# Kernel tuning notes

Hardware: AMD Instinct MI355X
Metric: run time of the kernel (lower is better)

Reference implementation:

```python
import jax, jax.numpy as jnp
import numpy as np

# Model dims
H = 1024          # hidden_size
I = 2048          # intermediate_size
E = 8             # num_experts
IE = I // E       # expert_intermediate_size = 256
V = 100000        # vocab_size
B, S = 8, 2048


def _rowwise_quantize(x):
    """Dynamic per-row int8 quantization (faithful to dynamic_quantize_int8, per_channel=True).
    Returns quantized values kept in float32 (identical values to int8->float cast) and per-row scale."""
    max_vals = jnp.max(jnp.abs(x), axis=-1, keepdims=True)
    scale = jnp.maximum(max_vals / 127.0, 1e-8)
    x_q = jnp.clip(jnp.round(x / scale), -128.0, 127.0)
    return x_q, scale[..., 0]


def _quantize_weight(w):
    """Per-output-channel int8 quantization of a [K, N] weight (as in from_float)."""
    max_vals = jnp.max(jnp.abs(w), axis=0, keepdims=True)      # [1, N]
    scale = jnp.maximum(max_vals / 127.0, 1e-8)
    w_q = jnp.clip(jnp.round(w / scale), -128.0, 127.0).astype(jnp.int8)
    return w_q, scale[0]


def setup_inputs() -> dict:
    key = jax.random.key(0)
    ks = jax.random.split(key, 6)
    hidden_states = jax.random.normal(ks[0], (B, S, H), dtype=jnp.float32)
    token_ids = jax.random.randint(ks[1], (B, S), 0, V, dtype=jnp.int32)

    # Pre-quantized expert weights (int8) with per-output-channel fp32 scales.
    gate_w = jax.random.normal(ks[2], (E, H, IE), dtype=jnp.float32) * 0.02
    up_w = jax.random.normal(ks[3], (E, H, IE), dtype=jnp.float32) * 0.02
    down_w = jax.random.normal(ks[4], (E, IE, H), dtype=jnp.float32) * 0.02
    gate_q, gate_scale = jax.vmap(_quantize_weight)(gate_w)   # [E,H,IE] int8, [E,IE]
    up_q, up_scale = jax.vmap(_quantize_weight)(up_w)         # [E,H,IE] int8, [E,IE]
    down_q, down_scale = jax.vmap(_quantize_weight)(down_w)   # [E,IE,H] int8, [E,H]

    # Deterministic contiguous token->expert mapping (V divisible by E here).
    token_to_expert = jnp.minimum(jnp.arange(V, dtype=jnp.int32) // (V // E), E - 1)

    return {
        "hidden_states": hidden_states,
        "token_ids": token_ids,
        "gate_q": gate_q, "gate_scale": gate_scale,
        "up_q": up_q, "up_scale": up_scale,
        "down_q": down_q, "down_scale": down_scale,
        "token_to_expert": token_to_expert,
    }


def reference(hidden_states, token_ids, gate_q, gate_scale, up_q, up_scale,
              down_q, down_scale, token_to_expert):
    Bh, Sh, Hh = hidden_states.shape
    n_exp = gate_q.shape[0]
    vocab = token_to_expert.shape[0]

    tid = jnp.clip(token_ids, 0, vocab - 1)
    expert_ids = token_to_expert[tid].reshape(-1)             # [T]

    x = hidden_states.reshape(-1, Hh)                          # [T, H]
    # Per-row activation quantization is expert-independent -> do it once for all tokens.
    x_q, x_s = _rowwise_quantize(x)                            # [T,H], [T]

    gq = gate_q.astype(jnp.float32)
    uq = up_q.astype(jnp.float32)
    dq = down_q.astype(jnp.float32)

    out = jnp.zeros_like(x)
    for e in range(n_exp):  # small fixed expert count
        # fused quantize-GEMM: int8 matmul + per-row activation scale + per-col weight scale
        gate = (x_q @ gq[e]) * x_s[:, None] * gate_scale[e][None, :]   # [T, IE]
        up = (x_q @ uq[e]) * x_s[:, None] * up_scale[e][None, :]       # [T, IE]
        inter = jax.nn.silu(gate) * up
        i_q, i_s = _rowwise_quantize(inter)
        o = (i_q @ dq[e]) * i_s[:, None] * down_scale[e][None, :]      # [T, H]
        out = jnp.where((expert_ids == e)[:, None], o, out)
    return out.reshape(Bh, Sh, Hh)
```

## Files before the change

kernel.cpp:

```cpp
#include <hip/hip_runtime.h>
#include <hip/hip_bf16.h>

typedef int   int4v   __attribute__((ext_vector_type(4)));
typedef float float4v __attribute__((ext_vector_type(4)));

#define T_TOK 16384
#define TPAD  16448
#define HD    1024
#define IE    256
#define EN    8
#define VSZ   100000

#define M_OFF 16
#define M_TS1 25
#define M_TS2 34

#define XQ_OFF   0ull
#define IQ_OFF   16842752ull
#define PB1_OFF  21053440ull
#define PB2_OFF  25247744ull
#define PERM_OFF 27344896ull
#define XS_OFF   27410688ull
#define IS_OFF   27476480ull
#define META_OFF 27542272ull
#define BC_OFF   27542528ull
#define BB_OFF   27544576ull

__global__ void k_hist(const int* __restrict__ ids, const int* __restrict__ t2e,
                       int* __restrict__ bc) {
    __shared__ int h[EN];
    if (threadIdx.x < EN) h[threadIdx.x] = 0;
    __syncthreads();
    int t = blockIdx.x * 256 + threadIdx.x;
    int id = ids[t]; id = min(max(id, 0), VSZ - 1);
    atomicAdd(&h[t2e[id]], 1);
    __syncthreads();
    if (threadIdx.x < EN) bc[blockIdx.x * EN + threadIdx.x] = h[threadIdx.x];
}

__global__ __launch_bounds__(512) void k_scan(const int* __restrict__ bc,
                                              int* __restrict__ bbase,
                                              int* __restrict__ meta) {
    int e = threadIdx.x >> 6;
    int b = threadIdx.x & 63;
    int c = bc[b * EN + e];
    int inc = c;
    #pragma unroll
    for (int s = 1; s < 64; s <<= 1) {
        int v = __shfl_up(inc, s, 64);
        if (b >= s) inc += v;
    }
    int exc = inc - c;
    __shared__ int tot[EN];
    __shared__ int goff[EN];
    if (b == 63) tot[e] = inc;
    __syncthreads();
    if (threadIdx.x == 0) {
        int off = 0, t1 = 0, t2 = 0;
        meta[M_OFF] = 0; meta[M_TS1] = 0; meta[M_TS2] = 0;
        #pragma unroll
        for (int i = 0; i < EN; ++i) {
            goff[i] = off;
            int cc = tot[i];
            off += cc; t1 += (cc + 63) >> 6; t2 += (cc + 31) >> 5;
            meta[M_OFF + i + 1] = off;
            meta[M_TS1 + i + 1] = t1;
            meta[M_TS2 + i + 1] = t2;
        }
    }
    __syncthreads();
    bbase[b * EN + e] = goff[e] + exc;
}

__global__ void k_assign(const int* __restrict__ ids, const int* __restrict__ t2e,
                         const int* __restrict__ bbase, int* __restrict__ perm) {
    __shared__ int cur[EN];
    if (threadIdx.x < EN) cur[threadIdx.x] = bbase[blockIdx.x * EN + threadIdx.x];
    __syncthreads();
    int t = blockIdx.x * 256 + threadIdx.x;
    int id = ids[t]; id = min(max(id, 0), VSZ - 1);
    int e = t2e[id];
    int slot = atomicAdd(&cur[e], 1);
    perm[slot] = t;
}

__global__ __launch_bounds__(256) void k_repack(const int* __restrict__ gq,
                                                const int* __restrict__ uq,
                                                const int* __restrict__ dq,
                                                signed char* __restrict__ pb1,
                                                signed char* __restrict__ pb2) {
    int idx = blockIdx.x * 256 + threadIdx.x;
    if (idx < 262144) {
        int n = idx & 511, kc = (idx >> 9) & 63, e = idx >> 15;
        const int* src = (n < 256) ? gq + (((size_t)((e << 10) + (kc << 4)) << 8) + n)
                                   : uq + (((size_t)((e << 10) + (kc << 4)) << 8) + (n - 256));
        int4v pk;
        #pragma unroll
        for (int jj = 0; jj < 4; ++jj) {
            int b0 = src[(size_t)(jj * 4 + 0) << 8], b1 = src[(size_t)(jj * 4 + 1) << 8];
            int b2 = src[(size_t)(jj * 4 + 2) << 8], b3 = src[(size_t)(jj * 4 + 3) << 8];
            pk[jj] = (b0 & 255) | ((b1 & 255) << 8) | ((b2 & 255) << 16) | (b3 << 24);
        }
        *(int4v*)(pb1 + ((size_t)((((e << 6) + kc) << 9) + n) << 4)) = pk;
    } else {
        int j = idx - 262144;
        int n = j & 1023, kc = (j >> 10) & 15, e = j >> 14;
        const int* src = dq + (((size_t)((e << 8) + (kc << 4)) << 10) + n);
        int4v pk;
        #pragma unroll
        for (int jj = 0; jj < 4; ++jj) {
            int b0 = src[(size_t)(jj * 4 + 0) << 10], b1 = src[(size_t)(jj * 4 + 1) << 10];
            int b2 = src[(size_t)(jj * 4 + 2) << 10], b3 = src[(size_t)(jj * 4 + 3) << 10];
            pk[jj] = (b0 & 255) | ((b1 & 255) << 8) | ((b2 & 255) << 16) | (b3 << 24);
        }
        *(int4v*)(pb2 + ((size_t)((((e << 4) + kc) << 10) + n) << 4)) = pk;
    }
}

__global__ __launch_bounds__(256) void k_quant(const float* __restrict__ hidden,
                                               const int* __restrict__ perm,
                                               signed char* __restrict__ xq,
                                               float* __restrict__ xs) {
    int w = threadIdx.x >> 6, lane = threadIdx.x & 63;
    int slot = blockIdx.x * 4 + w;
    int token = perm[slot];
    const float* row = hidden + (size_t)token * HD;
    float v[16];
    #pragma unroll
    for (int j = 0; j < 4; ++j) {
        float4v f = *(const float4v*)(row + lane * 16 + j * 4);
        v[j*4+0] = f[0]; v[j*4+1] = f[1]; v[j*4+2] = f[2]; v[j*4+3] = f[3];
    }
    float mx = 0.0f;
    #pragma unroll
    for (int j = 0; j < 16; ++j) mx = fmaxf(mx, fabsf(v[j]));
    #pragma unroll
    for (int s = 1; s < 64; s <<= 1) mx = fmaxf(mx, __shfl_xor(mx, s, 64));
    float sc = fmaxf(mx / 127.0f, 1e-8f);
    if (lane == 0) xs[slot] = sc;
    int4v pk;
    #pragma unroll
    for (int j = 0; j < 4; ++j) {
        int b[4];
        #pragma unroll
        for (int u = 0; u < 4; ++u) {
            float t = rintf(v[j*4+u] / sc);
            t = fminf(fmaxf(t, -128.0f), 127.0f);
            b[u] = (int)t;
        }
        pk[j] = (b[0] & 255) | ((b[1] & 255) << 8) | ((b[2] & 255) << 16) | (b[3] << 24);
    }
    *(int4v*)(xq + (size_t)slot * HD + lane * 16) = pk;
}

__global__ __launch_bounds__(256) void k_gemm1(const signed char* __restrict__ xq,
                                               const signed char* __restrict__ pb1,
                                               const float* __restrict__ xs,
                                               const float* __restrict__ gsc,
                                               const float* __restrict__ usc,
                                               const int* __restrict__ meta,
                                               signed char* __restrict__ iq,
                                               float* __restrict__ isc) {
    int b = blockIdx.x;
    int e = -1, m0 = 0, gend = 0;
    #pragma unroll
    for (int i = 0; i < EN; ++i) {
        int s0 = meta[M_TS1 + i], s1 = meta[M_TS1 + i + 1];
        if (b >= s0 && b < s1) { e = i; m0 = meta[M_OFF + i] + ((b - s0) << 6); gend = meta[M_OFF + i + 1]; }
    }
    if (e < 0) return;
    const int w = threadIdx.x >> 6, lane = threadIdx.x & 63;
    const int q = lane >> 4, r = lane & 15;

    int4v zero = {0, 0, 0, 0};
    int4v accg[4][4], accu[4][4];
    #pragma unroll
    for (int mi = 0; mi < 4; ++mi)
        #pragma unroll
        for (int i = 0; i < 4; ++i) { accg[mi][i] = zero; accu[mi][i] = zero; }

    const signed char* pbe = pb1 + (size_t)e * (64 * 512 * 16);
    for (int k0 = 0; k0 < HD; k0 += 64) {
        int4v a[4];
        #pragma unroll
        for (int mi = 0; mi < 4; ++mi)
            a[mi] = *(const int4v*)(xq + (size_t)(m0 + mi * 16 + r) * HD + k0 + q * 16);
        int kc = (k0 >> 4) + q;
        #pragma unroll
        for (int i = 0; i < 4; ++i) {
            int n = w * 64 + i * 16 + r;
            int4v bg = *(const int4v*)(pbe + (((size_t)kc * 512 + n) << 4));
            int4v bu = *(const int4v*)(pbe + (((size_t)kc * 512 + n + 256) << 4));
            #pragma unroll
            for (int mi = 0; mi < 4; ++mi) {
                accg[mi][i] = __builtin_amdgcn_mfma_i32_16x16x64_i8(a[mi], bg, accg[mi][i], 0, 0, 0);
                accu[mi][i] = __builtin_amdgcn_mfma_i32_16x16x64_i8(a[mi], bu, accu[mi][i], 0, 0, 0);
            }
        }
    }

    float gs[4], us[4];
    #pragma unroll
    for (int i = 0; i < 4; ++i) {
        int n = w * 64 + i * 16 + r;
        gs[i] = gsc[e * IE + n];
        us[i] = usc[e * IE + n];
    }
    float xsr[4][4];
    #pragma unroll
    for (int mi = 0; mi < 4; ++mi)
        #pragma unroll
        for (int g = 0; g < 4; ++g)
            xsr[mi][g] = xs[m0 + mi * 16 + q * 4 + g];

    float inter[4][4][4];
    float pm[4][4];
    #pragma unroll
    for (int mi = 0; mi < 4; ++mi)
        #pragma unroll
        for (int g = 0; g < 4; ++g) {
            float mx = 0.0f;
            #pragma unroll
            for (int i = 0; i < 4; ++i) {
                float gv = (float)accg[mi][i][g] * xsr[mi][g] * gs[i];
                float uv = (float)accu[mi][i][g] * xsr[mi][g] * us[i];
                float sg = gv / (1.0f + expf(-gv));
                float vv = sg * uv;
                inter[mi][i][g] = vv;
                mx = fmaxf(mx, fabsf(vv));
            }
            #pragma unroll
            for (int s = 1; s < 16; s <<= 1) mx = fmaxf(mx, __shfl_xor(mx, s, 64));
            pm[mi][g] = mx;
        }

    __shared__ float pmax[4][64];
    __shared__ float rsc[64];
    if (r == 0) {
        #pragma unroll
        for (int mi = 0; mi < 4; ++mi)
            #pragma unroll
            for (int g = 0; g < 4; ++g)
                pmax[w][mi * 16 + q * 4 + g] = pm[mi][g];
    }
    __syncthreads();
    if (threadIdx.x < 64) {
        int row = threadIdx.x;
        float mx = fmaxf(fmaxf(pmax[0][row], pmax[1][row]), fmaxf(pmax[2][row], pmax[3][row]));
        float sc = fmaxf(mx / 127.0f, 1e-8f);
        rsc[row] = sc;
        if (m0 + row < gend) isc[m0 + row] = sc;
    }
    __syncthreads();
    #pragma unroll
    for (int mi = 0; mi < 4; ++mi)
        #pragma unroll
        for (int g = 0; g < 4; ++g) {
            int row = mi * 16 + q * 4 + g;
            int slot = m0 + row;
            if (slot < gend) {
                float sc = rsc[row];
                #pragma unroll
                for (int i = 0; i < 4; ++i) {
                    float t = rintf(inter[mi][i][g] / sc);
                    t = fminf(fmaxf(t, -128.0f), 127.0f);
                    iq[(size_t)slot * IE + w * 64 + i * 16 + r] = (signed char)(int)t;
                }
            }
        }
}

__global__ __launch_bounds__(256) void k_gemm2(const signed char* __restrict__ iq,
                                               const signed char* __restrict__ pb2,
                                               const float* __restrict__ isc,
                                               const float* __restrict__ dsc,
                                               const int* __restrict__ meta,
                                               const int* __restrict__ perm,
                                               float* __restrict__ out) {
    int b = blockIdx.x;
    int e = -1, m0 = 0, gend = 0;
    #pragma unroll
    for (int i = 0; i < EN; ++i) {
        int s0 = meta[M_TS2 + i], s1 = meta[M_TS2 + i + 1];
        if (b >= s0 && b < s1) { e = i; m0 = meta[M_OFF + i] + ((b - s0) << 5); gend = meta[M_OFF + i + 1]; }
    }
    if (e < 0) return;
    const int w = threadIdx.x >> 6, lane = threadIdx.x & 63;
    const int q = lane >> 4, r = lane & 15;

    int4v zero = {0, 0, 0, 0};
    int4v acc[2][16];
    #pragma unroll
    for (int mi = 0; mi < 2; ++mi)
        #pragma unroll
        for (int i = 0; i < 16; ++i) acc[mi][i] = zero;

    const signed char* pbe = pb2 + (size_t)e * (16 * 1024 * 16);
    for (int k0 = 0; k0 < IE; k0 += 64) {
        int4v a[2];
        #pragma unroll
        for (int mi = 0; mi < 2; ++mi)
            a[mi] = *(const int4v*)(iq + (size_t)(m0 + mi * 16 + r) * IE + k0 + q * 16);
        int kc = (k0 >> 4) + q;
        #pragma unroll
        for (int i = 0; i < 16; ++i) {
            int n = w * 256 + i * 16 + r;
            int4v bb = *(const int4v*)(pbe + (((size_t)kc * 1024 + n) << 4));
            acc[0][i] = __builtin_amdgcn_mfma_i32_16x16x64_i8(a[0], bb, acc[0][i], 0, 0, 0);
            acc[1][i] = __builtin_amdgcn_mfma_i32_16x16x64_i8(a[1], bb, acc[1][i], 0, 0, 0);
        }
    }

    float ds[16];
    #pragma unroll
    for (int i = 0; i < 16; ++i)
        ds[i] = dsc[e * HD + w * 256 + i * 16 + r];
    float isr[2][4]; int tok[2][4];
    #pragma unroll
    for (int mi = 0; mi < 2; ++mi)
        #pragma unroll
        for (int g = 0; g < 4; ++g) {
            int slot = m0 + mi * 16 + q * 4 + g;
            isr[mi][g] = isc[slot];
            tok[mi][g] = perm[slot];
        }
    #pragma unroll
    for (int mi = 0; mi < 2; ++mi)
        #pragma unroll
        for (int g = 0; g < 4; ++g) {
            int slot = m0 + mi * 16 + q * 4 + g;
            if (slot < gend) {
                float vs = isr[mi][g];
                size_t ob = (size_t)tok[mi][g] * HD + w * 256 + r;
                #pragma unroll
                for (int i = 0; i < 16; ++i)
                    out[ob + i * 16] = (float)acc[mi][i][g] * vs * ds[i];
            }
        }
}

extern "C" void kernel_launch(void* const* d_in, const int* in_sizes, int n_in,
                              void* d_out, int out_size, void* d_ws, size_t ws_size,
                              hipStream_t stream) {
    const float* hidden = (const float*)d_in[0];
    const int*   ids    = (const int*)d_in[1];
    const int*   gq     = (const int*)d_in[2];
    const float* gsc    = (const float*)d_in[3];
    const int*   uq     = (const int*)d_in[4];
    const float* usc    = (const float*)d_in[5];
    const int*   dq     = (const int*)d_in[6];
    const float* dsc    = (const float*)d_in[7];
    const int*   t2e    = (const int*)d_in[8];
    float* out = (float*)d_out;

    char* ws = (char*)d_ws;
    signed char* xq  = (signed char*)(ws + XQ_OFF);
    signed char* iq  = (signed char*)(ws + IQ_OFF);
    signed char* pb1 = (signed char*)(ws + PB1_OFF);
    signed char* pb2 = (signed char*)(ws + PB2_OFF);
    int*   perm = (int*)(ws + PERM_OFF);
    float* xs   = (float*)(ws + XS_OFF);
    float* isc  = (float*)(ws + IS_OFF);
    int*   meta = (int*)(ws + META_OFF);
    int*   bc   = (int*)(ws + BC_OFF);
    int*   bbase= (int*)(ws + BB_OFF);

    k_hist<<<64, 256, 0, stream>>>(ids, t2e, bc);
    k_scan<<<1, 512, 0, stream>>>(bc, bbase, meta);
    k_assign<<<64, 256, 0, stream>>>(ids, t2e, bbase, perm);
    k_repack<<<1536, 256, 0, stream>>>(gq, uq, dq, pb1, pb2);
    k_quant<<<4096, 256, 0, stream>>>(hidden, perm, xq, xs);
    k_gemm1<<<264, 256, 0, stream>>>(xq, pb1, xs, gsc, usc, meta, iq, isc);
    k_gemm2<<<520, 256, 0, stream>>>(iq, pb2, isc, dsc, meta, perm, out);
}
```

Baseline: 249.4 us.

## Stage GEMM operands through double-buffered LDS via direct global-to-LDS loads

After: 211.4 us. 15.2% less time.

```diff
diff --git a/kernel.cpp b/kernel.cpp
--- a/kernel.cpp
+++ b/kernel.cpp
@@ -25,6 +25,13 @@
 #define META_OFF 27542272ull
 #define BC_OFF   27542528ull
 #define BB_OFF   27544576ull
+
+__device__ __forceinline__ void gload16(const void* g, void* l) {
+    __builtin_amdgcn_global_load_lds(
+        (const __attribute__((address_space(1))) unsigned int*)g,
+        (__attribute__((address_space(3))) unsigned int*)l,
+        16, 0, 0);
+}
 
 __global__ void k_hist(const int* __restrict__ ids, const int* __restrict__ t2e,
                        int* __restrict__ bc) {
@@ -153,14 +160,14 @@
     *(int4v*)(xq + (size_t)slot * HD + lane * 16) = pk;
 }
 
-__global__ __launch_bounds__(256) void k_gemm1(const signed char* __restrict__ xq,
-                                               const signed char* __restrict__ pb1,
-                                               const float* __restrict__ xs,
-                                               const float* __restrict__ gsc,
-                                               const float* __restrict__ usc,
-                                               const int* __restrict__ meta,
-                                               signed char* __restrict__ iq,
-                                               float* __restrict__ isc) {
+__global__ __launch_bounds__(256, 2) void k_gemm1(const signed char* __restrict__ xq,
+                                                  const signed char* __restrict__ pb1,
+                                                  const float* __restrict__ xs,
+                                                  const float* __restrict__ gsc,
+                                                  const float* __restrict__ usc,
+                                                  const int* __restrict__ meta,
+                                                  signed char* __restrict__ iq,
+                                                  float* __restrict__ isc) {
     int b = blockIdx.x;
     int e = -1, m0 = 0, gend = 0;
     #pragma unroll
@@ -172,6 +179,28 @@
     const int w = threadIdx.x >> 6, lane = threadIdx.x & 63;
     const int q = lane >> 4, r = lane & 15;
 
+    __shared__ signed char lB[2][32768];
+    __shared__ signed char lA[2][4096];
+    __shared__ float pmax[4][64];
+    __shared__ float rsc[64];
+
+    const signed char* pbe = pb1 + (size_t)e * (64 * 512 * 16);
+    const int arow = (w << 4) + (lane >> 2);
+    const int acq  = (lane & 3) ^ ((lane >> 2) & 3);
+    const signed char* ga_base = xq + (size_t)(m0 + arow) * HD + (acq << 4);
+
+    #define G1_STAGE(buf, kt)                                                          \
+        {                                                                              \
+            int kc0 = (kt) << 2;                                                       \
+            _Pragma("unroll")                                                          \
+            for (int j = 0; j < 8; ++j) {                                              \
+                int n = ((j << 6) + lane) ^ ((w & 1) << 3);                            \
+                gload16(pbe + (((size_t)(kc0 + w) * 512 + n) << 4),                    \
+                        &lB[buf][((w << 3) + j) << 10]);                               \
+            }                                                                          \
+            gload16(ga_base + ((kt) << 6), &lA[buf][w << 10]);                         \
+        }
+
     int4v zero = {0, 0, 0, 0};
     int4v accg[4][4], accu[4][4];
     #pragma unroll
@@ -179,30 +208,36 @@
         #pragma unroll
         for (int i = 0; i < 4; ++i) { accg[mi][i] = zero; accu[mi][i] = zero; }
 
-    const signed char* pbe = pb1 + (size_t)e * (64 * 512 * 16);
-    for (int k0 = 0; k0 < HD; k0 += 64) {
+    G1_STAGE(0, 0);
+    for (int kt = 0; kt < 16; ++kt) {
+        int cur = kt & 1;
+        if (kt < 15) G1_STAGE(cur ^ 1, kt + 1);
+        __syncthreads();
         int4v a[4];
         #pragma unroll
         for (int mi = 0; mi < 4; ++mi)
-            a[mi] = *(const int4v*)(xq + (size_t)(m0 + mi * 16 + r) * HD + k0 + q * 16);
-        int kc = (k0 >> 4) + q;
+            a[mi] = *(const int4v*)&lA[cur][(((mi << 4) + r) << 6) + ((q ^ (r & 3)) << 4)];
         #pragma unroll
         for (int i = 0; i < 4; ++i) {
-            int n = w * 64 + i * 16 + r;
-            int4v bg = *(const int4v*)(pbe + (((size_t)kc * 512 + n) << 4));
-            int4v bu = *(const int4v*)(pbe + (((size_t)kc * 512 + n + 256) << 4));
+            int n = (w << 6) + (i << 4) + r;
+            int sg = (q << 9) + (n ^ ((q & 1) << 3));
+            int su = (q << 9) + ((n + 256) ^ ((q & 1) << 3));
+            int4v bg = *(const int4v*)&lB[cur][sg << 4];
+            int4v bu = *(const int4v*)&lB[cur][su << 4];
             #pragma unroll
             for (int mi = 0; mi < 4; ++mi) {
                 accg[mi][i] = __builtin_amdgcn_mfma_i32_16x16x64_i8(a[mi], bg, accg[mi][i], 0, 0, 0);
                 accu[mi][i] = __builtin_amdgcn_mfma_i32_16x16x64_i8(a[mi], bu, accu[mi][i], 0, 0, 0);
             }
         }
-    }
+        __syncthreads();
+    }
+    #undef G1_STAGE
 
     float gs[4], us[4];
     #pragma unroll
     for (int i = 0; i < 4; ++i) {
-        int n = w * 64 + i * 16 + r;
+        int n = (w << 6) + (i << 4) + r;
         gs[i] = gsc[e * IE + n];
         us[i] = usc[e * IE + n];
     }
@@ -234,8 +269,6 @@
             pm[mi][g] = mx;
         }
 
-    __shared__ float pmax[4][64];
-    __shared__ float rsc[64];
     if (r == 0) {
         #pragma unroll
         for (int mi = 0; mi < 4; ++mi)
@@ -264,57 +297,82 @@
                 for (int i = 0; i < 4; ++i) {
                     float t = rintf(inter[mi][i][g] / sc);
                     t = fminf(fmaxf(t, -128.0f), 127.0f);
-                    iq[(size_t)slot * IE + w * 64 + i * 16 + r] = (signed char)(int)t;
+                    iq[(size_t)slot * IE + (w << 6) + (i << 4) + r] = (signed char)(int)t;
                 }
             }
         }
 }
 
-__global__ __launch_bounds__(256) void k_gemm2(const signed char* __restrict__ iq,
-                                               const signed char* __restrict__ pb2,
-                                               const float* __restrict__ isc,
-                                               const float* __restrict__ dsc,
-                                               const int* __restrict__ meta,
-                                               const int* __restrict__ perm,
-                                               float* __restrict__ out) {
-    int b = blockIdx.x;
+__global__ __launch_bounds__(256, 2) void k_gemm2(const signed char* __restrict__ iq,
+                                                  const signed char* __restrict__ pb2,
+                                                  const float* __restrict__ isc,
+                                                  const float* __restrict__ dsc,
+                                                  const int* __restrict__ meta,
+                                                  const int* __restrict__ perm,
+                                                  float* __restrict__ out) {
+    int tile = blockIdx.x >> 1, nh = blockIdx.x & 1;
     int e = -1, m0 = 0, gend = 0;
     #pragma unroll
     for (int i = 0; i < EN; ++i) {
         int s0 = meta[M_TS2 + i], s1 = meta[M_TS2 + i + 1];
-        if (b >= s0 && b < s1) { e = i; m0 = meta[M_OFF + i] + ((b - s0) << 5); gend = meta[M_OFF + i + 1]; }
+        if (tile >= s0 && tile < s1) { e = i; m0 = meta[M_OFF + i] + ((tile - s0) << 5); gend = meta[M_OFF + i + 1]; }
     }
     if (e < 0) return;
     const int w = threadIdx.x >> 6, lane = threadIdx.x & 63;
     const int q = lane >> 4, r = lane & 15;
 
+    __shared__ signed char lB[2][32768];
+    __shared__ signed char lA[2][2048];
+
+    const signed char* pbe = pb2 + (size_t)e * (16 * 1024 * 16);
+    const int arow = (w << 4) + (lane >> 2);
+    const int acq  = (lane & 3) ^ ((lane >> 2) & 3);
+    const signed char* ga_base = iq + (size_t)(m0 + arow) * IE + (acq << 4);
+
+    #define G2_STAGE(buf, kt)                                                          \
+        {                                                                              \
+            int kc0 = (kt) << 2;                                                       \
+            _Pragma("unroll")                                                          \
+            for (int j = 0; j < 8; ++j) {                                              \
+                int n = ((j << 6) + lane) ^ ((w & 1) << 3);                            \
+                gload16(pbe + (((size_t)(kc0 + w) * 1024 + (nh << 9) + n) << 4),       \
+                        &lB[buf][((w << 3) + j) << 10]);                               \
+            }                                                                          \
+            if (w < 2) gload16(ga_base + ((kt) << 6), &lA[buf][w << 10]);              \
+        }
+
     int4v zero = {0, 0, 0, 0};
-    int4v acc[2][16];
+    int4v acc[2][8];
     #pragma unroll
     for (int mi = 0; mi < 2; ++mi)
         #pragma unroll
-        for (int i = 0; i < 16; ++i) acc[mi][i] = zero;
-
-    const signed char* pbe = pb2 + (size_t)e * (16 * 1024 * 16);
-    for (int k0 = 0; k0 < IE; k0 += 64) {
+        for (int i = 0; i < 8; ++i) acc[mi][i] = zero;
+
+    G2_STAGE(0, 0);
+    for (int kt = 0; kt < 4; ++kt) {
+        int cur = kt & 1;
+        if (kt < 3) G2_STAGE(cur ^ 1, kt + 1);
+        __syncthreads();
         int4v a[2];
         #pragma unroll
         for (int mi = 0; mi < 2; ++mi)
-            a[mi] = *(const int4v*)(iq + (size_t)(m0 + mi * 16 + r) * IE + k0 + q * 16);
-        int kc = (k0 >> 4) + q;
-        #pragma unroll
-        for (int i = 0; i < 16; ++i) {
-            int n = w * 256 + i * 16 + r;
-            int4v bb = *(const int4v*)(pbe + (((size_t)kc * 1024 + n) << 4));
+            a[mi] = *(const int4v*)&lA[cur][(((mi << 4) + r) << 6) + ((q ^ (r & 3)) << 4)];
+        #pragma unroll
+        for (int i = 0; i < 8; ++i) {
+            int n = (w << 7) + (i << 4) + r;
+            int sb = (q << 9) + (n ^ ((q & 1) << 3));
+            int4v bb = *(const int4v*)&lB[cur][sb << 4];
             acc[0][i] = __builtin_amdgcn_mfma_i32_16x16x64_i8(a[0], bb, acc[0][i], 0, 0, 0);
             acc[1][i] = __builtin_amdgcn_mfma_i32_16x16x64_i8(a[1], bb, acc[1][i], 0, 0, 0);
         }
-    }
-
-    float ds[16];
-    #pragma unroll
-    for (int i = 0; i < 16; ++i)
-        ds[i] = dsc[e * HD + w * 256 + i * 16 + r];
+        __syncthreads();
+    }
+    #undef G2_STAGE
+
+    float ds[8];
+    #pragma unroll
+    for (int i = 0; i < 8; ++i)
+        ds[i] = dsc[e * HD + (nh << 9) + (w << 7) + (i << 4) + r];
     float isr[2][4]; int tok[2][4];
     #pragma unroll
     for (int mi = 0; mi < 2; ++mi)
@@ -331,10 +389,10 @@
             int slot = m0 + mi * 16 + q * 4 + g;
             if (slot < gend) {
                 float vs = isr[mi][g];
-                size_t ob = (size_t)tok[mi][g] * HD + w * 256 + r;
+                size_t ob = (size_t)tok[mi][g] * HD + (nh << 9) + (w << 7) + r;
                 #pragma unroll
-                for (int i = 0; i < 16; ++i)
-                    out[ob + i * 16] = (float)acc[mi][i][g] * vs * ds[i];
+                for (int i = 0; i < 8; ++i)
+                    out[ob + (i << 4)] = (float)acc[mi][i][g] * vs * ds[i];
             }
         }
 }
@@ -371,5 +429,5 @@
     k_repack<<<1536, 256, 0, stream>>>(gq, uq, dq, pb1, pb2);
     k_quant<<<4096, 256, 0, stream>>>(hidden, perm, xq, xs);
     k_gemm1<<<264, 256, 0, stream>>>(xq, pb1, xs, gsc, usc, meta, iq, isc);
-    k_gemm2<<<520, 256, 0, stream>>>(iq, pb2, isc, dsc, meta, perm, out);
-}
+    k_gemm2<<<1040, 256, 0, stream>>>(iq, pb2, isc, dsc, meta, perm, out);
+}
```

## Quantize tokens in natural order, gather in GEMM1, pipeline loads, split GEMM2 N

Applied to the files above, without the earlier changes.

Result: faster. 241.3 us (-3.2%).

```diff
diff --git a/kernel.cpp b/kernel.cpp
--- a/kernel.cpp
+++ b/kernel.cpp
@@ -118,12 +118,10 @@
 }
 
 __global__ __launch_bounds__(256) void k_quant(const float* __restrict__ hidden,
-                                               const int* __restrict__ perm,
                                                signed char* __restrict__ xq,
                                                float* __restrict__ xs) {
     int w = threadIdx.x >> 6, lane = threadIdx.x & 63;
-    int slot = blockIdx.x * 4 + w;
-    int token = perm[slot];
+    int token = blockIdx.x * 4 + w;
     const float* row = hidden + (size_t)token * HD;
     float v[16];
     #pragma unroll
@@ -137,7 +135,7 @@
     #pragma unroll
     for (int s = 1; s < 64; s <<= 1) mx = fmaxf(mx, __shfl_xor(mx, s, 64));
     float sc = fmaxf(mx / 127.0f, 1e-8f);
-    if (lane == 0) xs[slot] = sc;
+    if (lane == 0) xs[token] = sc;
     int4v pk;
     #pragma unroll
     for (int j = 0; j < 4; ++j) {
@@ -150,7 +148,7 @@
         }
         pk[j] = (b[0] & 255) | ((b[1] & 255) << 8) | ((b[2] & 255) << 16) | (b[3] << 24);
     }
-    *(int4v*)(xq + (size_t)slot * HD + lane * 16) = pk;
+    *(int4v*)(xq + (size_t)token * HD + lane * 16) = pk;
 }
 
 __global__ __launch_bounds__(256) void k_gemm1(const signed char* __restrict__ xq,
@@ -159,6 +157,7 @@
                                                const float* __restrict__ gsc,
                                                const float* __restrict__ usc,
                                                const int* __restrict__ meta,
+                                               const int* __restrict__ perm,
                                                signed char* __restrict__ iq,
                                                float* __restrict__ isc) {
     int b = blockIdx.x;
@@ -172,6 +171,26 @@
     const int w = threadIdx.x >> 6, lane = threadIdx.x & 63;
     const int q = lane >> 4, r = lane & 15;
 
+    const signed char* pbe = pb1 + (size_t)e * (64 * 512 * 16);
+    const signed char* arow[4];
+    #pragma unroll
+    for (int mi = 0; mi < 4; ++mi)
+        arow[mi] = xq + (size_t)perm[min(m0 + (mi << 4) + r, T_TOK - 1)] * HD + (q << 4);
+    const signed char* brow = pbe + (((size_t)q * 512 + (w << 6) + r) << 4);
+
+    int4v A[2][4], BG[2][4], BU[2][4];
+    #define G1_LOAD(buf, kt)                                                            \
+        {                                                                               \
+            _Pragma("unroll")                                                           \
+            for (int mi = 0; mi < 4; ++mi)                                              \
+                A[buf][mi] = *(const int4v*)(arow[mi] + ((kt) << 6));                   \
+            _Pragma("unroll")                                                           \
+            for (int i = 0; i < 4; ++i) {                                               \
+                BG[buf][i] = *(const int4v*)(brow + ((size_t)(kt) << 15) + (i << 8));   \
+                BU[buf][i] = *(const int4v*)(brow + ((size_t)(kt) << 15) + (i << 8) + 4096); \
+            }                                                                           \
+        }
+
     int4v zero = {0, 0, 0, 0};
     int4v accg[4][4], accu[4][4];
     #pragma unroll
@@ -179,30 +198,26 @@
         #pragma unroll
         for (int i = 0; i < 4; ++i) { accg[mi][i] = zero; accu[mi][i] = zero; }
 
-    const signed char* pbe = pb1 + (size_t)e * (64 * 512 * 16);
-    for (int k0 = 0; k0 < HD; k0 += 64) {
-        int4v a[4];
-        #pragma unroll
-        for (int mi = 0; mi < 4; ++mi)
-            a[mi] = *(const int4v*)(xq + (size_t)(m0 + mi * 16 + r) * HD + k0 + q * 16);
-        int kc = (k0 >> 4) + q;
+    G1_LOAD(0, 0);
+    #pragma unroll
+    for (int kt = 0; kt < 16; ++kt) {
+        int cur = kt & 1;
+        if (kt < 15) G1_LOAD(cur ^ 1, kt + 1);
         #pragma unroll
         for (int i = 0; i < 4; ++i) {
-            int n = w * 64 + i * 16 + r;
-            int4v bg = *(const int4v*)(pbe + (((size_t)kc * 512 + n) << 4));
-            int4v bu = *(const int4v*)(pbe + (((size_t)kc * 512 + n + 256) << 4));
             #pragma unroll
             for (int mi = 0; mi < 4; ++mi) {
-                accg[mi][i] = __builtin_amdgcn_mfma_i32_16x16x64_i8(a[mi], bg, accg[mi][i], 0, 0, 0);
-                accu[mi][i] = __builtin_amdgcn_mfma_i32_16x16x64_i8(a[mi], bu, accu[mi][i], 0, 0, 0);
+                accg[mi][i] = __builtin_amdgcn_mfma_i32_16x16x64_i8(A[cur][mi], BG[cur][i], accg[mi][i], 0, 0, 0);
+                accu[mi][i] = __builtin_amdgcn_mfma_i32_16x16x64_i8(A[cur][mi], BU[cur][i], accu[mi][i], 0, 0, 0);
             }
         }
     }
+    #undef G1_LOAD
 
     float gs[4], us[4];
     #pragma unroll
     for (int i = 0; i < 4; ++i) {
-        int n = w * 64 + i * 16 + r;
+        int n = (w << 6) + (i << 4) + r;
         gs[i] = gsc[e * IE + n];
         us[i] = usc[e * IE + n];
     }
@@ -210,8 +225,10 @@
     #pragma unroll
     for (int mi = 0; mi < 4; ++mi)
         #pragma unroll
-        for (int g = 0; g < 4; ++g)
-            xsr[mi][g] = xs[m0 + mi * 16 + q * 4 + g];
+        for (int g = 0; g < 4; ++g) {
+            int sl = min(m0 + mi * 16 + q * 4 + g, T_TOK - 1);
+            xsr[mi][g] = xs[perm[sl]];
+        }
 
     float inter[4][4][4];
     float pm[4][4];
@@ -264,7 +281,7 @@
                 for (int i = 0; i < 4; ++i) {
                     float t = rintf(inter[mi][i][g] / sc);
                     t = fminf(fmaxf(t, -128.0f), 127.0f);
-                    iq[(size_t)slot * IE + w * 64 + i * 16 + r] = (signed char)(int)t;
+                    iq[(size_t)slot * IE + (w << 6) + (i << 4) + r] = (signed char)(int)t;
                 }
             }
         }
@@ -277,44 +294,51 @@
                                                const int* __restrict__ meta,
                                                const int* __restrict__ perm,
                                                float* __restrict__ out) {
-    int b = blockIdx.x;
+    int tile = blockIdx.x >> 2, nt = blockIdx.x & 3;
     int e = -1, m0 = 0, gend = 0;
     #pragma unroll
     for (int i = 0; i < EN; ++i) {
         int s0 = meta[M_TS2 + i], s1 = meta[M_TS2 + i + 1];
-        if (b >= s0 && b < s1) { e = i; m0 = meta[M_OFF + i] + ((b - s0) << 5); gend = meta[M_OFF + i + 1]; }
+        if (tile >= s0 && tile < s1) { e = i; m0 = meta[M_OFF + i] + ((tile - s0) << 5); gend = meta[M_OFF + i + 1]; }
     }
     if (e < 0) return;
     const int w = threadIdx.x >> 6, lane = threadIdx.x & 63;
     const int q = lane >> 4, r = lane & 15;
 
+    const signed char* pbe = pb2 + (size_t)e * (16 * 1024 * 16);
+    const signed char* arow0 = iq + (size_t)(m0 + r) * IE + (q << 4);
+    const signed char* arow1 = arow0 + (size_t)16 * IE;
+    const signed char* bb = pbe + (((size_t)q * 1024 + (nt << 8) + (w << 6) + r) << 4);
+
+    int4v A0[4], A1[4], B[4][4];
+    #pragma unroll
+    for (int ks = 0; ks < 4; ++ks) {
+        A0[ks] = *(const int4v*)(arow0 + (ks << 6));
+        A1[ks] = *(const int4v*)(arow1 + (ks << 6));
+        #pragma unroll
+        for (int i = 0; i < 4; ++i)
+            B[ks][i] = *(const int4v*)(bb + ((size_t)ks << 16) + (i << 8));
+    }
+
     int4v zero = {0, 0, 0, 0};
-    int4v acc[2][16];
+    int4v acc[2][4];
     #pragma unroll
     for (int mi = 0; mi < 2; ++mi)
         #pragma unroll
-        for (int i = 0; i < 16; ++i) acc[mi][i] = zero;
-
-    const signed char* pbe = pb2 + (size_t)e * (16 * 1024 * 16);
-    for (int k0 = 0; k0 < IE; k0 += 64) {
-        int4v a[2];
-        #pragma unroll
-        for (int mi = 0; mi < 2; ++mi)
-            a[mi] = *(const int4v*)(iq + (size_t)(m0 + mi * 16 + r) * IE + k0 + q * 16);
-        int kc = (k0 >> 4) + q;
-        #pragma unroll
-        for (int i = 0; i < 16; ++i) {
-            int n = w * 256 + i * 16 + r;
-            int4v bb = *(const int4v*)(pbe + (((size_t)kc * 1024 + n) << 4));
-            acc[0][i] = __builtin_amdgcn_mfma_i32_16x16x64_i8(a[0], bb, acc[0][i], 0, 0, 0);
-            acc[1][i] = __builtin_amdgcn_mfma_i32_16x16x64_i8(a[1], bb, acc[1][i], 0, 0, 0);
-        }
-    }
-
-    float ds[16];
-    #pragma unroll
-    for (int i = 0; i < 16; ++i)
-        ds[i] = dsc[e * HD + w * 256 + i * 16 + r];
+        for (int i = 0; i < 4; ++i) acc[mi][i] = zero;
+
+    #pragma unroll
+    for (int ks = 0; ks < 4; ++ks)
+        #pragma unroll
+        for (int i = 0; i < 4; ++i) {
+            acc[0][i] = __builtin_amdgcn_mfma_i32_16x16x64_i8(A0[ks], B[ks][i], acc[0][i], 0, 0, 0);
+            acc[1][i] = __builtin_amdgcn_mfma_i32_16x16x64_i8(A1[ks], B[ks][i], acc[1][i], 0, 0, 0);
+        }
+
+    float ds[4];
+    #pragma unroll
+    for (int i = 0; i < 4; ++i)
+        ds[i] = dsc[e * HD + (nt << 8) + (w << 6) + (i << 4) + r];
     float isr[2][4]; int tok[2][4];
     #pragma unroll
     for (int mi = 0; mi < 2; ++mi)
@@ -322,7 +346,7 @@
         for (int g = 0; g < 4; ++g) {
             int slot = m0 + mi * 16 + q * 4 + g;
             isr[mi][g] = isc[slot];
-            tok[mi][g] = perm[slot];
+            tok[mi][g] = perm[min(slot, T_TOK - 1)];
         }
     #pragma unroll
     for (int mi = 0; mi < 2; ++mi)
@@ -331,10 +355,10 @@
             int slot = m0 + mi * 16 + q * 4 + g;
             if (slot < gend) {
                 float vs = isr[mi][g];
-                size_t ob = (size_t)tok[mi][g] * HD + w * 256 + r;
+                size_t ob = (size_t)tok[mi][g] * HD + (nt << 8) + (w << 6) + r;
                 #pragma unroll
-                for (int i = 0; i < 16; ++i)
-                    out[ob + i * 16] = (float)acc[mi][i][g] * vs * ds[i];
+                for (int i = 0; i < 4; ++i)
+                    out[ob + (i << 4)] = (float)acc[mi][i][g] * vs * ds[i];
             }
         }
 }
@@ -369,7 +393,7 @@
     k_scan<<<1, 512, 0, stream>>>(bc, bbase, meta);
     k_assign<<<64, 256, 0, stream>>>(ids, t2e, bbase, perm);
     k_repack<<<1536, 256, 0, stream>>>(gq, uq, dq, pb1, pb2);
-    k_quant<<<4096, 256, 0, stream>>>(hidden, perm, xq, xs);
-    k_gemm1<<<264, 256, 0, stream>>>(xq, pb1, xs, gsc, usc, meta, iq, isc);
-    k_gemm2<<<520, 256, 0, stream>>>(iq, pb2, isc, dsc, meta, perm, out);
-}
+    k_quant<<<4096, 256, 0, stream>>>(hidden, xq, xs);
+    k_gemm1<<<264, 256, 0, stream>>>(xq, pb1, xs, gsc, usc, meta, perm, iq, isc);
+    k_gemm2<<<2080, 256, 0, stream>>>(iq, pb2, isc, dsc, meta, perm, out);
+}
```
